# Optimization experiments

Hardware: AMD Instinct MI355X
Metric: run time of the kernel (lower is better)

The kernel has to match this reference:

```python
import jax, jax.numpy as jnp
import numpy as np

D_MODEL = 1024
D_HEAD = 64
M_BITS = 32


def setup_inputs() -> dict:
    key = jax.random.key(0)
    ks = jax.random.split(key, 6)
    B, N, M = 2, 2048, 2048
    Q = jax.random.normal(ks[0], (B, N, D_MODEL), dtype=jnp.float32)
    K = jax.random.normal(ks[1], (B, M, D_MODEL), dtype=jnp.float32)
    V = jax.random.normal(ks[2], (B, M, D_MODEL), dtype=jnp.float32)
    s = 1.0 / np.sqrt(D_MODEL)
    Wq = jax.random.normal(ks[3], (D_MODEL, M_BITS), dtype=jnp.float32) * s
    Wk = jax.random.normal(ks[4], (D_MODEL, M_BITS), dtype=jnp.float32) * s
    Wv = jax.random.normal(ks[5], (D_MODEL, D_HEAD), dtype=jnp.float32) * s
    temperature = jnp.ones((1,), dtype=jnp.float32)
    return {"Q": Q, "K": K, "V": V, "Wq": Wq, "Wk": Wk, "Wv": Wv,
            "temperature": temperature}


def tropical_matmul(A, Bt):
    # A: [B, N, m], Bt: [B, M, m] (already transposed form of [B, m, M])
    # (A \odot B)_{ij} = min_k (A_ik + B_kj)
    return jnp.min(A[:, :, None, :] + Bt[:, None, :, :], axis=-1)  # [B, N, M]


def reference(Q, K, V, Wq, Wk, Wv, temperature):
    # REWA tropical encoders (continuous): linear projections to m_bits
    Qt = jnp.einsum('bnd,dm->bnm', Q, Wq)   # [B, N, m_bits]
    Kt = jnp.einsum('bsd,dm->bsm', K, Wk)   # [B, M, m_bits]
    Vp = jnp.einsum('bsd,dh->bsh', V, Wv)   # [B, M, d_head]
    # tropical (min-plus) scores, negated so shorter paths score higher
    scores = -tropical_matmul(Qt, Kt)       # [B, N, M]
    scores = scores / jax.nn.softplus(temperature[0])
    attn = jax.nn.softmax(scores, axis=-1)  # [B, N, M]
    out = jnp.einsum('bnm,bmh->bnh', attn, Vp)  # [B, N, d_head]
    return out, attn
```

## Files before the change

### kernel.cpp

```cpp
#include <hip/hip_runtime.h>
#include <math.h>

#define DM 1024
#define NB 2048
#define MBITS 32
#define DH 64

typedef __attribute__((ext_vector_type(4))) float floatx4;
typedef __attribute__((ext_vector_type(8))) short shortx8;

__device__ __forceinline__ unsigned short f32_to_bf16(float f) {
    union { float f; unsigned u; } v; v.f = f;
    unsigned r = v.u + 0x7FFF + ((v.u >> 16) & 1);
    return (unsigned short)(r >> 16);
}

__device__ __forceinline__ void split2(float x0, float x1, unsigned& hp, unsigned& lp) {
    union { float f; unsigned u; } a, b; a.f = x0; b.f = x1;
    unsigned h0 = a.u & 0xFFFF0000u, h1 = b.u & 0xFFFF0000u;
    union { unsigned u; float f; } hf0, hf1; hf0.u = h0; hf1.u = h1;
    union { float f; unsigned u; } c, d;
    c.f = x0 - hf0.f;
    d.f = x1 - hf1.f;
    hp = (h0 >> 16) | h1;
    lp = (c.u >> 16) | (d.u & 0xFFFF0000u);
}

__global__ __launch_bounds__(256) void wprep_kernel(
    const float* __restrict__ Wq, const float* __restrict__ Wk,
    const float* __restrict__ Wv, unsigned short* __restrict__ Wf)
{
    int wv = blockIdx.x * 4 + (threadIdx.x >> 6);
    int l  = threadIdx.x & 63;
    const float* W; int C, kc32, ct;
    if (wv < 64)       { W = Wq; C = 32; kc32 = wv >> 1;  ct = wv & 1; }
    else if (wv < 128) { W = Wk; C = 32; int z = wv - 64;  kc32 = z >> 1; ct = z & 1; }
    else               { W = Wv; C = 64; int z = wv - 128; kc32 = z >> 2; ct = z & 3; }
    int k0 = kc32 * 32 + (l >> 4) * 8;
    int c  = ct * 16 + (l & 15);
    float x[8];
    #pragma unroll
    for (int j = 0; j < 8; ++j) x[j] = W[(size_t)(k0 + j) * C + c];
    unsigned hp[4], lp[4];
    #pragma unroll
    for (int j2 = 0; j2 < 4; ++j2) split2(x[2 * j2], x[2 * j2 + 1], hp[j2], lp[j2]);
    uint4 hv; hv.x = hp[0]; hv.y = hp[1]; hv.z = hp[2]; hv.w = hp[3];
    uint4 lv; lv.x = lp[0]; lv.y = lp[1]; lv.z = lp[2]; lv.w = lp[3];
    *(uint4*)&Wf[(size_t)wv * 1024 + l * 8]       = hv;
    *(uint4*)&Wf[(size_t)wv * 1024 + 512 + l * 8] = lv;
}

__global__ __launch_bounds__(256) void proj_mfma2_kernel(
    const float* __restrict__ Q, const float* __restrict__ K, const float* __restrict__ V,
    const unsigned short* __restrict__ Wf,
    float* __restrict__ Qt, float* __restrict__ Kt, unsigned short* __restrict__ VpT)
{
    __shared__ float red[4][64][16];

    int gb = blockIdx.x;
    int job = gb >> 8, tile = gb & 255;
    int r0 = tile * 16;
    const float* X = (job == 0) ? Q : (job == 1) ? K : V;
    int ntct  = (job == 2) ? 4 : 2;
    int pbase = job << 6;
    int t = threadIdx.x, w = t >> 6, l = t & 63;
    int lrow = l & 15, lq = l >> 4;

    const float* xrow = &X[(size_t)(r0 + lrow) * DM + w * 256 + lq * 8];

    floatx4 acc[4];
    #pragma unroll
    for (int i = 0; i < 4; ++i) acc[i] = (floatx4){0.f, 0.f, 0.f, 0.f};

    #pragma unroll
    for (int s = 0; s < 8; ++s) {
        floatx4 g0 = *(const floatx4*)(xrow + s * 32);
        floatx4 g1 = *(const floatx4*)(xrow + s * 32 + 4);
        union { unsigned u[4]; shortx8 v; } ahi, alo;
        split2(g0.x, g0.y, ahi.u[0], alo.u[0]);
        split2(g0.z, g0.w, ahi.u[1], alo.u[1]);
        split2(g1.x, g1.y, ahi.u[2], alo.u[2]);
        split2(g1.z, g1.w, ahi.u[3], alo.u[3]);
        int kc32 = w * 8 + s;
        #pragma unroll
        for (int ct = 0; ct < 4; ++ct) {
            if (ct >= ntct) break;
            int p = pbase + kc32 * ntct + ct;
            const unsigned short* wp = &Wf[(size_t)p * 1024 + l * 8];
            shortx8 bhi = *(const shortx8*)wp;
            shortx8 blo = *(const shortx8*)(wp + 512);
            acc[ct] = __builtin_amdgcn_mfma_f32_16x16x32_bf16(ahi.v, bhi, acc[ct], 0, 0, 0);
            acc[ct] = __builtin_amdgcn_mfma_f32_16x16x32_bf16(ahi.v, blo, acc[ct], 0, 0, 0);
            acc[ct] = __builtin_amdgcn_mfma_f32_16x16x32_bf16(alo.v, bhi, acc[ct], 0, 0, 0);
        }
    }

    #pragma unroll
    for (int ct = 0; ct < 4; ++ct) {
        if (ct >= ntct) break;
        #pragma unroll
        for (int r = 0; r < 4; ++r) red[w][l][ct * 4 + r] = acc[ct][r];
    }
    __syncthreads();

    int row = r0 + lq * 4 + w;
    if (job < 2) {
        float* Y = (job == 0) ? Qt : Kt;
        #pragma unroll
        for (int ct = 0; ct < 2; ++ct) {
            float v = red[0][l][ct * 4 + w] + red[1][l][ct * 4 + w]
                    + red[2][l][ct * 4 + w] + red[3][l][ct * 4 + w];
            Y[(size_t)row * MBITS + ct * 16 + lrow] = v;
        }
    } else {
        int b = row >> 11, j = row & 2047;
        #pragma unroll
        for (int ct = 0; ct < 4; ++ct) {
            float v = red[0][l][ct * 4 + w] + red[1][l][ct * 4 + w]
                    + red[2][l][ct * 4 + w] + red[3][l][ct * 4 + w];
            VpT[(size_t)b * (DH * NB) + (size_t)(ct * 16 + lrow) * NB + j] = f32_to_bf16(v);
        }
    }
}

template <typename ET>
__global__ __launch_bounds__(256) void trop_score_kernel(
    const float* __restrict__ Qt, const float* __restrict__ Kt,
    const float* __restrict__ temp, float* __restrict__ partial,
    ET* __restrict__ ebuf)
{
    __shared__ float Qs[16][36];
    __shared__ float Ks[256][36];

    int b  = blockIdx.z;
    int jc = blockIdx.y;
    int i0 = blockIdx.x * 16;
    int t  = threadIdx.x;
    int w  = t >> 6, l = t & 63;

    if (t < 128) {
        int row = t >> 3, k4 = t & 7;
        *(floatx4*)&Qs[row][k4 * 4] =
            *(const floatx4*)&Qt[(size_t)(b * NB + i0 + row) * MBITS + k4 * 4];
    }
    #pragma unroll
    for (int u = 0; u < 8; ++u) {
        int flat4 = u * 256 + t;
        int row = flat4 >> 3, k4 = flat4 & 7;
        *(floatx4*)&Ks[row][k4 * 4] =
            *(const floatx4*)&Kt[(size_t)(b * NB + jc * 256 + row) * MBITS + k4 * 4];
    }
    float tv = temp[0];
    float c2 = -(1.0f / log1pf(__expf(tv))) * 1.44269504088896340736f;
    __syncthreads();

    float m[4][4];
    #pragma unroll
    for (int ii = 0; ii < 4; ++ii)
        #pragma unroll
        for (int jj = 0; jj < 4; ++jj) m[ii][jj] = 1e30f;

    #pragma unroll
    for (int k4 = 0; k4 < 8; ++k4) {
        floatx4 q[4], kk[4];
        #pragma unroll
        for (int ii = 0; ii < 4; ++ii) q[ii] = *(const floatx4*)&Qs[w + 4 * ii][k4 * 4];
        #pragma unroll
        for (int jj = 0; jj < 4; ++jj) kk[jj] = *(const floatx4*)&Ks[l + 64 * jj][k4 * 4];
        #pragma unroll
        for (int ii = 0; ii < 4; ++ii)
            #pragma unroll
            for (int jj = 0; jj < 4; ++jj) {
                float a0 = q[ii].x + kk[jj].x;
                float a1 = q[ii].y + kk[jj].y;
                float a2 = q[ii].z + kk[jj].z;
                float a3 = q[ii].w + kk[jj].w;
                m[ii][jj] = fminf(fminf(m[ii][jj], fminf(a0, a1)), fminf(a2, a3));
            }
    }

    float psum[4];
    #pragma unroll
    for (int ii = 0; ii < 4; ++ii) {
        int i = w + 4 * ii;
        float s = 0.f;
        #pragma unroll
        for (int jj = 0; jj < 4; ++jj) {
            int j = l + 64 * jj;
            float e = exp2f(c2 * m[ii][jj]);
            size_t idx = (size_t)(b * NB + i0 + i) * 2048 + jc * 256 + j;
            if (sizeof(ET) == 2) ebuf[idx] = (ET)f32_to_bf16(e);
            else                 ebuf[idx] = (ET)e;
            s += e;
        }
        psum[ii] = s;
    }

    #pragma unroll
    for (int ii = 0; ii < 4; ++ii) {
        float v = psum[ii];
        #pragma unroll
        for (int off = 1; off < 64; off <<= 1) v += __shfl_xor(v, off, 64);
        if (l == 0) partial[((size_t)b * NB + i0 + w + 4 * ii) * 8 + jc] = v;
    }
}

template <bool EBF16>
__global__ __launch_bounds__(256) void trop_out_kernel(
    const unsigned short* __restrict__ VpT, const float* __restrict__ partial,
    const void* __restrict__ ebuf_in, float* __restrict__ outp, float* __restrict__ attn)
{
    __shared__ unsigned short Vs[64][256];
    __shared__ unsigned short Es[16][264];
    __shared__ float inv_s[16];

    int b  = blockIdx.z;
    int jc = blockIdx.y;
    int i0 = blockIdx.x * 16;
    int t  = threadIdx.x;
    int w  = t >> 6, l = t & 63;

    #pragma unroll
    for (int u = 0; u < 8; ++u) {
        int flat16 = u * 256 + t;
        int h = flat16 >> 5, c = flat16 & 31;
        uint4 g = *(const uint4*)&VpT[(size_t)b * (DH * NB) + (size_t)h * NB + jc * 256 + c * 8];
        *(uint4*)&Vs[h][(c ^ (h & 31)) * 8] = g;
    }
    if (t < 16) {
        float s = 0.f;
        #pragma unroll
        for (int p = 0; p < 8; ++p) s += partial[((size_t)b * NB + i0 + t) * 8 + p];
        inv_s[t] = 1.0f / s;
    }

    if (EBF16) {
        const unsigned short* eb = (const unsigned short*)ebuf_in;
        #pragma unroll
        for (int u = 0; u < 2; ++u) {
            int flat = u * 256 + t;
            int row = flat >> 5, c = flat & 31;
            uint4 g = *(const uint4*)&eb[(size_t)(b * NB + i0 + row) * 2048 + jc * 256 + c * 8];
            *(uint4*)&Es[row][c * 8] = g;
        }
        __syncthreads();
        int row = t >> 4, cb = (t & 15) * 16;
        float iv = inv_s[row];
        #pragma unroll
        for (int h8 = 0; h8 < 2; ++h8) {
            uint4 e8 = *(const uint4*)&Es[row][cb + h8 * 8];
            unsigned uu[4] = {e8.x, e8.y, e8.z, e8.w};
            float f[8];
            #pragma unroll
            for (int z = 0; z < 4; ++z) {
                union { unsigned u; float f; } v0, v1;
                v0.u = uu[z] << 16; v1.u = uu[z] & 0xFFFF0000u;
                f[2 * z] = v0.f * iv; f[2 * z + 1] = v1.f * iv;
            }
            size_t gidx = (size_t)(b * NB + i0 + row) * 2048 + jc * 256 + cb + h8 * 8;
            floatx4 o0; o0.x = f[0]; o0.y = f[1]; o0.z = f[2]; o0.w = f[3];
            floatx4 o1; o1.x = f[4]; o1.y = f[5]; o1.z = f[6]; o1.w = f[7];
            *(floatx4*)&attn[gidx]     = o0;
            *(floatx4*)&attn[gidx + 4] = o1;
        }
    } else {
        __syncthreads();
        #pragma unroll
        for (int u = 0; u < 4; ++u) {
            int flat4 = u * 256 + t;
            int row = flat4 >> 6, c4 = flat4 & 63;
            size_t g = (size_t)(b * NB + i0 + row) * 2048 + jc * 256 + c4 * 4;
            floatx4 e4 = *(const floatx4*)&attn[g];
            float iv = inv_s[row];
            unsigned u0 = (unsigned)f32_to_bf16(e4.x) | ((unsigned)f32_to_bf16(e4.y) << 16);
            unsigned u1 = (unsigned)f32_to_bf16(e4.z) | ((unsigned)f32_to_bf16(e4.w) << 16);
            uint2 pk; pk.x = u0; pk.y = u1;
            *(uint2*)&Es[row][c4 * 4] = pk;
            e4.x *= iv; e4.y *= iv; e4.z *= iv; e4.w *= iv;
            *(floatx4*)&attn[g] = e4;
        }
    }
    __syncthreads();

    floatx4 acc = {0.f, 0.f, 0.f, 0.f};
    #pragma unroll
    for (int kk = 0; kk < 8; ++kk) {
        int mrow = l & 15, q4 = l >> 4;
        shortx8 a = *(const shortx8*)&Es[mrow][kk * 32 + q4 * 8];
        int h = w * 16 + mrow;
        int c = kk * 4 + q4;
        shortx8 bf = *(const shortx8*)&Vs[h][(c ^ (h & 31)) * 8];
        acc = __builtin_amdgcn_mfma_f32_16x16x32_bf16(a, bf, acc, 0, 0, 0);
    }

    #pragma unroll
    for (int r = 0; r < 4; ++r) {
        int irow = (l >> 4) * 4 + r;
        atomicAdd(&outp[(size_t)(b * NB + i0 + irow) * DH + w * 16 + (l & 15)],
                  acc[r] * inv_s[irow]);
    }
}

extern "C" void kernel_launch(void* const* d_in, const int* in_sizes, int n_in,
                              void* d_out, int out_size, void* d_ws, size_t ws_size,
                              hipStream_t stream) {
    (void)in_sizes; (void)n_in; (void)out_size;
    const float* Q    = (const float*)d_in[0];
    const float* K    = (const float*)d_in[1];
    const float* V    = (const float*)d_in[2];
    const float* Wq   = (const float*)d_in[3];
    const float* Wk   = (const float*)d_in[4];
    const float* Wv   = (const float*)d_in[5];
    const float* temp = (const float*)d_in[6];

    float* outp = (float*)d_out;
    float* attn = outp + 2 * 2048 * 64;

    char* ws = (char*)d_ws;
    float*          Qt      = (float*)(ws);
    float*          Kt      = (float*)(ws + 524288);
    float*          partial = (float*)(ws + 1048576);
    unsigned short* Wf      = (unsigned short*)(ws + 1179648);
    unsigned short* VpT     = (unsigned short*)(ws + 1703936);
    unsigned short* Ebuf    = (unsigned short*)(ws + 2228224);
    bool bf16path = ws_size >= (size_t)2228224 + 16777216;

    hipMemsetAsync(d_out, 0, 262144 * sizeof(float), stream);

    wprep_kernel<<<64, 256, 0, stream>>>(Wq, Wk, Wv, Wf);
    proj_mfma2_kernel<<<768, 256, 0, stream>>>(Q, K, V, Wf, Qt, Kt, VpT);

    if (bf16path) {
        trop_score_kernel<unsigned short><<<dim3(128, 8, 2), 256, 0, stream>>>(
            Qt, Kt, temp, partial, Ebuf);
        trop_out_kernel<true><<<dim3(128, 8, 2), 256, 0, stream>>>(
            VpT, partial, Ebuf, outp, attn);
    } else {
        trop_score_kernel<float><<<dim3(128, 8, 2), 256, 0, stream>>>(
            Qt, Kt, temp, partial, attn);
        trop_out_kernel<false><<<dim3(128, 8, 2), 256, 0, stream>>>(
            VpT, partial, attn, outp, attn);
    }
}
```

Before: 155.4 us.

## Recompute tropical scores in output kernel instead of storing bf16 exp buffer

The score kernel now only computes per-row partial softmax sums. A fused kernel recomputes the min-plus scores and exponentials, writes the normalized attention directly and feeds a bf16 copy to the MFMA for the output. This removes the 16 MB intermediate exp buffer write and read, at the cost of doing the tropical min-plus computation twice. The V tile is now loaded straight from global memory into MFMA operands instead of through shared memory, and the projection kernel software-prefetches the next input chunk.

```diff
diff --git a/kernel.cpp b/kernel.cpp
--- a/kernel.cpp
+++ b/kernel.cpp
@@ -72,10 +72,16 @@
     #pragma unroll
     for (int i = 0; i < 4; ++i) acc[i] = (floatx4){0.f, 0.f, 0.f, 0.f};
 
+    floatx4 g0 = *(const floatx4*)(xrow);
+    floatx4 g1 = *(const floatx4*)(xrow + 4);
+
     #pragma unroll
     for (int s = 0; s < 8; ++s) {
-        floatx4 g0 = *(const floatx4*)(xrow + s * 32);
-        floatx4 g1 = *(const floatx4*)(xrow + s * 32 + 4);
+        floatx4 n0, n1;
+        if (s < 7) {
+            n0 = *(const floatx4*)(xrow + (s + 1) * 32);
+            n1 = *(const floatx4*)(xrow + (s + 1) * 32 + 4);
+        }
         union { unsigned u[4]; shortx8 v; } ahi, alo;
         split2(g0.x, g0.y, ahi.u[0], alo.u[0]);
         split2(g0.z, g0.w, ahi.u[1], alo.u[1]);
@@ -93,6 +99,7 @@
             acc[ct] = __builtin_amdgcn_mfma_f32_16x16x32_bf16(ahi.v, blo, acc[ct], 0, 0, 0);
             acc[ct] = __builtin_amdgcn_mfma_f32_16x16x32_bf16(alo.v, bhi, acc[ct], 0, 0, 0);
         }
+        g0 = n0; g1 = n1;
     }
 
     #pragma unroll
@@ -123,11 +130,9 @@
     }
 }
 
-template <typename ET>
-__global__ __launch_bounds__(256) void trop_score_kernel(
+__global__ __launch_bounds__(256) void trop_sum_kernel(
     const float* __restrict__ Qt, const float* __restrict__ Kt,
-    const float* __restrict__ temp, float* __restrict__ partial,
-    ET* __restrict__ ebuf)
+    const float* __restrict__ temp, float* __restrict__ partial)
 {
     __shared__ float Qs[16][36];
     __shared__ float Ks[256][36];
@@ -179,38 +184,24 @@
             }
     }
 
-    float psum[4];
     #pragma unroll
     for (int ii = 0; ii < 4; ++ii) {
-        int i = w + 4 * ii;
-        float s = 0.f;
-        #pragma unroll
-        for (int jj = 0; jj < 4; ++jj) {
-            int j = l + 64 * jj;
-            float e = exp2f(c2 * m[ii][jj]);
-            size_t idx = (size_t)(b * NB + i0 + i) * 2048 + jc * 256 + j;
-            if (sizeof(ET) == 2) ebuf[idx] = (ET)f32_to_bf16(e);
-            else                 ebuf[idx] = (ET)e;
-            s += e;
-        }
-        psum[ii] = s;
-    }
-
-    #pragma unroll
-    for (int ii = 0; ii < 4; ++ii) {
-        float v = psum[ii];
-        #pragma unroll
-        for (int off = 1; off < 64; off <<= 1) v += __shfl_xor(v, off, 64);
-        if (l == 0) partial[((size_t)b * NB + i0 + w + 4 * ii) * 8 + jc] = v;
-    }
-}
-
-template <bool EBF16>
-__global__ __launch_bounds__(256) void trop_out_kernel(
-    const unsigned short* __restrict__ VpT, const float* __restrict__ partial,
-    const void* __restrict__ ebuf_in, float* __restrict__ outp, float* __restrict__ attn)
+        float s = exp2f(c2 * m[ii][0]) + exp2f(c2 * m[ii][1])
+                + exp2f(c2 * m[ii][2]) + exp2f(c2 * m[ii][3]);
+        #pragma unroll
+        for (int off = 1; off < 64; off <<= 1) s += __shfl_xor(s, off, 64);
+        if (l == 0) partial[((size_t)b * NB + i0 + w + 4 * ii) * 8 + jc] = s;
+    }
+}
+
+__global__ __launch_bounds__(256) void trop_fused_kernel(
+    const float* __restrict__ Qt, const float* __restrict__ Kt,
+    const unsigned short* __restrict__ VpT,
+    const float* __restrict__ temp, const float* __restrict__ partial,
+    float* __restrict__ outp, float* __restrict__ attn)
 {
-    __shared__ unsigned short Vs[64][256];
+    __shared__ float Qs[16][36];
+    __shared__ float Ks[256][36];
     __shared__ unsigned short Es[16][264];
     __shared__ float inv_s[16];
 
@@ -220,12 +211,17 @@
     int t  = threadIdx.x;
     int w  = t >> 6, l = t & 63;
 
+    if (t < 128) {
+        int row = t >> 3, k4 = t & 7;
+        *(floatx4*)&Qs[row][k4 * 4] =
+            *(const floatx4*)&Qt[(size_t)(b * NB + i0 + row) * MBITS + k4 * 4];
+    }
     #pragma unroll
     for (int u = 0; u < 8; ++u) {
-        int flat16 = u * 256 + t;
-        int h = flat16 >> 5, c = flat16 & 31;
-        uint4 g = *(const uint4*)&VpT[(size_t)b * (DH * NB) + (size_t)h * NB + jc * 256 + c * 8];
-        *(uint4*)&Vs[h][(c ^ (h & 31)) * 8] = g;
+        int flat4 = u * 256 + t;
+        int row = flat4 >> 3, k4 = flat4 & 7;
+        *(floatx4*)&Ks[row][k4 * 4] =
+            *(const floatx4*)&Kt[(size_t)(b * NB + jc * 256 + row) * MBITS + k4 * 4];
     }
     if (t < 16) {
         float s = 0.f;
@@ -233,63 +229,58 @@
         for (int p = 0; p < 8; ++p) s += partial[((size_t)b * NB + i0 + t) * 8 + p];
         inv_s[t] = 1.0f / s;
     }
-
-    if (EBF16) {
-        const unsigned short* eb = (const unsigned short*)ebuf_in;
-        #pragma unroll
-        for (int u = 0; u < 2; ++u) {
-            int flat = u * 256 + t;
-            int row = flat >> 5, c = flat & 31;
-            uint4 g = *(const uint4*)&eb[(size_t)(b * NB + i0 + row) * 2048 + jc * 256 + c * 8];
-            *(uint4*)&Es[row][c * 8] = g;
-        }
-        __syncthreads();
-        int row = t >> 4, cb = (t & 15) * 16;
-        float iv = inv_s[row];
-        #pragma unroll
-        for (int h8 = 0; h8 < 2; ++h8) {
-            uint4 e8 = *(const uint4*)&Es[row][cb + h8 * 8];
-            unsigned uu[4] = {e8.x, e8.y, e8.z, e8.w};
-            float f[8];
+    float tv = temp[0];
+    float c2 = -(1.0f / log1pf(__expf(tv))) * 1.44269504088896340736f;
+    __syncthreads();
+
+    float m[4][4];
+    #pragma unroll
+    for (int ii = 0; ii < 4; ++ii)
+        #pragma unroll
+        for (int jj = 0; jj < 4; ++jj) m[ii][jj] = 1e30f;
+
+    #pragma unroll
+    for (int k4 = 0; k4 < 8; ++k4) {
+        floatx4 q[4], kk[4];
+        #pragma unroll
+        for (int ii = 0; ii < 4; ++ii) q[ii] = *(const floatx4*)&Qs[w + 4 * ii][k4 * 4];
+        #pragma unroll
+        for (int jj = 0; jj < 4; ++jj) kk[jj] = *(const floatx4*)&Ks[l + 64 * jj][k4 * 4];
+        #pragma unroll
+        for (int ii = 0; ii < 4; ++ii)
             #pragma unroll
-            for (int z = 0; z < 4; ++z) {
-                union { unsigned u; float f; } v0, v1;
-                v0.u = uu[z] << 16; v1.u = uu[z] & 0xFFFF0000u;
-                f[2 * z] = v0.f * iv; f[2 * z + 1] = v1.f * iv;
+            for (int jj = 0; jj < 4; ++jj) {
+                float a0 = q[ii].x + kk[jj].x;
+                float a1 = q[ii].y + kk[jj].y;
+                float a2 = q[ii].z + kk[jj].z;
+                float a3 = q[ii].w + kk[jj].w;
+                m[ii][jj] = fminf(fminf(m[ii][jj], fminf(a0, a1)), fminf(a2, a3));
             }
-            size_t gidx = (size_t)(b * NB + i0 + row) * 2048 + jc * 256 + cb + h8 * 8;
-            floatx4 o0; o0.x = f[0]; o0.y = f[1]; o0.z = f[2]; o0.w = f[3];
-            floatx4 o1; o1.x = f[4]; o1.y = f[5]; o1.z = f[6]; o1.w = f[7];
-            *(floatx4*)&attn[gidx]     = o0;
-            *(floatx4*)&attn[gidx + 4] = o1;
-        }
-    } else {
-        __syncthreads();
-        #pragma unroll
-        for (int u = 0; u < 4; ++u) {
-            int flat4 = u * 256 + t;
-            int row = flat4 >> 6, c4 = flat4 & 63;
-            size_t g = (size_t)(b * NB + i0 + row) * 2048 + jc * 256 + c4 * 4;
-            floatx4 e4 = *(const floatx4*)&attn[g];
-            float iv = inv_s[row];
-            unsigned u0 = (unsigned)f32_to_bf16(e4.x) | ((unsigned)f32_to_bf16(e4.y) << 16);
-            unsigned u1 = (unsigned)f32_to_bf16(e4.z) | ((unsigned)f32_to_bf16(e4.w) << 16);
-            uint2 pk; pk.x = u0; pk.y = u1;
-            *(uint2*)&Es[row][c4 * 4] = pk;
-            e4.x *= iv; e4.y *= iv; e4.z *= iv; e4.w *= iv;
-            *(floatx4*)&attn[g] = e4;
+    }
+
+    #pragma unroll
+    for (int ii = 0; ii < 4; ++ii) {
+        int i = w + 4 * ii;
+        float iv = inv_s[i];
+        #pragma unroll
+        for (int jj = 0; jj < 4; ++jj) {
+            int j = l + 64 * jj;
+            float e = exp2f(c2 * m[ii][jj]);
+            attn[(size_t)(b * NB + i0 + i) * 2048 + jc * 256 + j] = e * iv;
+            Es[i][j] = f32_to_bf16(e);
         }
     }
     __syncthreads();
 
+    const unsigned short* vb =
+        &VpT[(size_t)b * (DH * NB) + (size_t)(w * 16 + (l & 15)) * NB
+             + jc * 256 + (l >> 4) * 8];
     floatx4 acc = {0.f, 0.f, 0.f, 0.f};
     #pragma unroll
     for (int kk = 0; kk < 8; ++kk) {
         int mrow = l & 15, q4 = l >> 4;
-        shortx8 a = *(const shortx8*)&Es[mrow][kk * 32 + q4 * 8];
-        int h = w * 16 + mrow;
-        int c = kk * 4 + q4;
-        shortx8 bf = *(const shortx8*)&Vs[h][(c ^ (h & 31)) * 8];
+        shortx8 a  = *(const shortx8*)&Es[mrow][kk * 32 + q4 * 8];
+        shortx8 bf = *(const shortx8*)(vb + kk * 32);
         acc = __builtin_amdgcn_mfma_f32_16x16x32_bf16(a, bf, acc, 0, 0, 0);
     }
 
@@ -304,7 +295,7 @@
 extern "C" void kernel_launch(void* const* d_in, const int* in_sizes, int n_in,
                               void* d_out, int out_size, void* d_ws, size_t ws_size,
                               hipStream_t stream) {
-    (void)in_sizes; (void)n_in; (void)out_size;
+    (void)in_sizes; (void)n_in; (void)out_size; (void)ws_size;
     const float* Q    = (const float*)d_in[0];
     const float* K    = (const float*)d_in[1];
     const float* V    = (const float*)d_in[2];
@@ -322,23 +313,12 @@
     float*          partial = (float*)(ws + 1048576);
     unsigned short* Wf      = (unsigned short*)(ws + 1179648);
     unsigned short* VpT     = (unsigned short*)(ws + 1703936);
-    unsigned short* Ebuf    = (unsigned short*)(ws + 2228224);
-    bool bf16path = ws_size >= (size_t)2228224 + 16777216;
 
     hipMemsetAsync(d_out, 0, 262144 * sizeof(float), stream);
 
     wprep_kernel<<<64, 256, 0, stream>>>(Wq, Wk, Wv, Wf);
     proj_mfma2_kernel<<<768, 256, 0, stream>>>(Q, K, V, Wf, Qt, Kt, VpT);
-
-    if (bf16path) {
-        trop_score_kernel<unsigned short><<<dim3(128, 8, 2), 256, 0, stream>>>(
-            Qt, Kt, temp, partial, Ebuf);
-        trop_out_kernel<true><<<dim3(128, 8, 2), 256, 0, stream>>>(
-            VpT, partial, Ebuf, outp, attn);
-    } else {
-        trop_score_kernel<float><<<dim3(128, 8, 2), 256, 0, stream>>>(
-            Qt, Kt, temp, partial, attn);
-        trop_out_kernel<false><<<dim3(128, 8, 2), 256, 0, stream>>>(
-            VpT, partial, attn, outp, attn);
-    }
-}
+    trop_sum_kernel<<<dim3(128, 8, 2), 256, 0, stream>>>(Qt, Kt, temp, partial);
+    trop_fused_kernel<<<dim3(128, 8, 2), 256, 0, stream>>>(
+        Qt, Kt, VpT, temp, partial, outp, attn);
+}
```

After: 161.2 us. 1.04x slower.
